# Optimization experiments

Measured on AMD Instinct MI355X. Metric: run time of the kernel, lower is better.

## Reference

```python
import jax, jax.numpy as jnp
import numpy as np
from jax import lax
from math import sqrt

POLE = sqrt(3.0) - 2.0                       # cubic B-spline pole
GAIN = (1.0 - POLE) * (1.0 - 1.0 / POLE)     # = 6.0
UPSAMPLING_FACTOR = 2


def _cubic_spline_1d(t):
    a = jnp.abs(t)
    out = (2.0 / 3.0 + (0.5 * a - 1.0) * a ** 2) * (a < 1)
    out = out + (-(a - 2.0) ** 3 / 6.0) * ((a >= 1) & (a < 2))
    return out


def _bspline_kernel(f):
    is_odd = f % 2
    k = 4 * f - is_odd
    start = (1 + is_odd) / (2 * f) - 2.0
    pts = jnp.arange(k, dtype=jnp.float32) * (1.0 / f) + start
    return _cubic_spline_1d(pts)


def _prefilter_1d(x, axis):
    """Causal + anticausal recursive cubic-spline coefficient filter along `axis`."""
    n = x.shape[axis]
    if n == 1:
        return x
    p = POLE
    xm = jnp.moveaxis(x * GAIN, axis, 0)  # (n, ...)
    i = np.arange(n)
    pows = jnp.asarray(p ** i + p ** (2 * n - 1 - i), dtype=x.dtype)
    # causal boundary condition (mirror)
    c0 = jnp.tensordot(pows, xm, axes=(0, 0)) * (p / (1.0 - p ** (2 * n))) + xm[0]

    def causal(carry, xi):
        y = xi + p * carry
        return y, y

    _, ys = lax.scan(causal, c0, xm[1:])
    cm = jnp.concatenate([c0[None], ys], axis=0)
    # anticausal boundary condition
    last = cm[-1] * (p / (p - 1.0))

    def anti(carry, ci):
        y = p * (carry - ci)
        return y, y

    _, ys2 = lax.scan(anti, last, cm[:-1], reverse=True)
    out = jnp.concatenate([ys2, last[None]], axis=0)
    return jnp.moveaxis(out, 0, axis)


def _upsample_1d(x, axis, kernel, f):
    """Strided transposed conv along `axis` with replicate padding of 2 (per-channel)."""
    dim_size = x.shape[axis]
    xm = jnp.moveaxis(x, axis, -1)
    lead = xm.shape[:-1]
    x3 = xm.reshape(-1, 1, dim_size)
    x3 = jnp.pad(x3, ((0, 0), (0, 0), (2, 2)), mode='edge')
    k = kernel.shape[0]
    implicit_padding = 7 * f // 2
    pad = k - 1 - implicit_padding  # conv_transpose == lhs-dilated correlation w/ flipped kernel
    out = lax.conv_general_dilated(
        x3,
        kernel[::-1][None, None, :],
        window_strides=(1,),
        padding=[(pad, pad)],
        lhs_dilation=(f,),
        dimension_numbers=('NCH', 'OIH', 'NCH'),
    )
    out = out.reshape(lead + (out.shape[-1],))
    return jnp.moveaxis(out, -1, axis)


def setup_inputs() -> dict:
    key = jax.random.key(0)
    volume = jax.random.normal(key, (2, 3, 96, 96, 96), dtype=jnp.float32)
    return {"volume": volume}


def reference(volume):
    f = UPSAMPLING_FACTOR
    kernel = _bspline_kernel(f).astype(volume.dtype)
    first_spatial_dim = min(volume.ndim - 1, 2)
    x = volume
    for axis in range(first_spatial_dim, volume.ndim):
        x = _prefilter_1d(x, axis)
    for axis in range(first_spatial_dim, volume.ndim):
        x = _upsample_1d(x, axis, kernel, f)
    return x
```

## Files before the change

kernel.cpp:

```cpp
#include <hip/hip_runtime.h>


#define TAPS 28

struct MTab { float v[192 * TAPS]; };

static constexpr MTab make_M() {
    const double p = -0.26794919243112270647253365849413;
    double pw[193] = {};
    pw[0] = 1.0;
    for (int i = 1; i <= 192; ++i) pw[i] = pw[i - 1] * p;
    double Wd[96][96] = {};
    for (int j = 0; j < 96; ++j) {
        double c[96] = {};
        double K = p / (1.0 - pw[192]);
        double cur = 6.0 * K * (pw[j] + pw[191 - j]) + (j == 0 ? 6.0 : 0.0);
        c[0] = cur;
        for (int i = 1; i < 96; ++i) {
            cur = (i == j ? 6.0 : 0.0) + p * cur;
            c[i] = cur;
        }
        double nxt = cur * (p / (p - 1.0));
        Wd[95][j] = nxt;
        for (int i = 94; i >= 0; --i) {
            nxt = p * (nxt - c[i]);
            Wd[i][j] = nxt;
        }
    }
    MTab M = {};
    const double cw[8] = {1.0 / 384.0, 121.0 / 384.0, 235.0 / 384.0, 27.0 / 384.0,
                          27.0 / 384.0, 235.0 / 384.0, 121.0 / 384.0, 1.0 / 384.0};
    for (int i = 0; i < 192; ++i) {
        int ph = i & 1;
        int cc = i >> 1;
        for (int t = 0; t < TAPS; ++t) {
            int j = cc - 13 + t;
            double m = 0.0;
            if (j >= 0 && j < 96) {
                for (int tt = 0; tt < 4; ++tt) {
                    int k = cc + ph - 2 + tt;
                    k = k < 0 ? 0 : (k > 95 ? 95 : k);
                    m += cw[ph * 4 + tt] * Wd[k][j];
                }
            }
            M.v[i * TAPS + t] = (float)m;
        }
    }
    return M;
}

static constexpr MTab h_M = make_M();
__device__ __constant__ MTab g_M = h_M;

__device__ alignas(16) float g_bufA[6 * 96 * 96 * 192];
__device__ alignas(16) float g_bufB[6 * 96 * 192 * 192];

__device__ __forceinline__ int clamp96(int j) { return j < 0 ? 0 : (j > 95 ? 95 : j); }

__global__ __launch_bounds__(512) void pass_z(const float* __restrict__ in,
                                              float* __restrict__ out) {
    __shared__ float s_in[64 * 97];
    __shared__ float s_out[64 * 193];
    const float* Mb = g_M.v;
    float w0[TAPS], w1[TAPS];
#pragma unroll
    for (int t = 0; t < TAPS; ++t) {
        w0[t] = Mb[96 * TAPS + t];
        w1[t] = Mb[97 * TAPS + t];
    }
    size_t base = (size_t)blockIdx.x * 64;
    const float* src = in + base * 96;
    int tid = threadIdx.x;
    for (int k = tid; k < 64 * 96; k += 512)
        s_in[(k / 96) * 97 + (k % 96)] = src[k];
    __syncthreads();

    int lane = tid & 63;
    int wave = tid >> 6;
    int c0 = wave * 12;
    const float* xl = s_in + lane * 97;
    float* op = s_out + lane * 193 + 2 * c0;
    float win[39];
#pragma unroll
    for (int k = 0; k < 39; ++k) win[k] = xl[clamp96(c0 - 13 + k)];

    if (wave >= 1 && wave <= 6) {
#pragma unroll
        for (int mi = 0; mi < 12; ++mi) {
            float a0 = 0.f, a1 = 0.f;
#pragma unroll
            for (int t = 0; t < TAPS; ++t) {
                float xv = win[mi + t];
                a0 = fmaf(w0[t], xv, a0);
                a1 = fmaf(w1[t], xv, a1);
            }
            op[2 * mi] = a0;
            op[2 * mi + 1] = a1;
        }
    } else {
#pragma unroll
        for (int mi = 0; mi < 12; ++mi) {
            int m = c0 + mi;
            int wb = __builtin_amdgcn_readfirstlane(m * 2 * TAPS);
            const float* wr = Mb + wb;
            float a0 = 0.f, a1 = 0.f;
#pragma unroll
            for (int t = 0; t < TAPS; ++t) {
                float xv = win[mi + t];
                a0 = fmaf(wr[t], xv, a0);
                a1 = fmaf(wr[TAPS + t], xv, a1);
            }
            op[2 * mi] = a0;
            op[2 * mi + 1] = a1;
        }
    }
    __syncthreads();
    float* dst = out + base * 192;
    for (int k = tid; k < 64 * 192; k += 512)
        dst[k] = s_out[(k / 192) * 193 + (k % 192)];
}

template <int INNER>
__global__ __launch_bounds__(256) void pass_staged(const float* __restrict__ in,
                                                   float* __restrict__ out) {
    constexpr int CT = INNER / 64;
    __shared__ float s[96 * 64];
    const float* Mb = g_M.v;
    int tid = threadIdx.x;
    int ct = blockIdx.x % CT;
    int o = blockIdx.x / CT;
    const float* src = in + (size_t)o * 96 * INNER + (size_t)ct * 64;
    float* dst = out + (size_t)o * 192 * INNER + (size_t)ct * 64;

#pragma unroll
    for (int it = 0; it < 6; ++it) {
        int k = tid + it * 256;
        int row = k >> 4;
        int c4 = k & 15;
        float4 v = *(const float4*)(src + (size_t)row * INNER + c4 * 4);
        *(float4*)(&s[row * 64 + c4 * 4]) = v;
    }
    __syncthreads();

    int col = tid & 63;
    int cq = tid >> 6;
    int c0 = cq * 24;

    float win[51];
#pragma unroll
    for (int k = 0; k < 51; ++k) win[k] = s[clamp96(c0 - 13 + k) * 64 + col];

    if (cq == 1 || cq == 2) {
        float w0[TAPS], w1[TAPS];
#pragma unroll
        for (int t = 0; t < TAPS; ++t) {
            w0[t] = Mb[96 * TAPS + t];
            w1[t] = Mb[97 * TAPS + t];
        }
#pragma unroll
        for (int mi = 0; mi < 24; ++mi) {
            float a0 = 0.f, a1 = 0.f;
#pragma unroll
            for (int t = 0; t < TAPS; ++t) {
                float xv = win[mi + t];
                a0 = fmaf(w0[t], xv, a0);
                a1 = fmaf(w1[t], xv, a1);
            }
            int m = c0 + mi;
            dst[(size_t)(2 * m) * INNER + col] = a0;
            dst[(size_t)(2 * m + 1) * INNER + col] = a1;
        }
    } else {
#pragma unroll
        for (int mi = 0; mi < 24; ++mi) {
            int m = c0 + mi;
            int wb = __builtin_amdgcn_readfirstlane(m * 2 * TAPS);
            const float* wr = Mb + wb;
            float a0 = 0.f, a1 = 0.f;
#pragma unroll
            for (int t = 0; t < TAPS; ++t) {
                float xv = win[mi + t];
                a0 = fmaf(wr[t], xv, a0);
                a1 = fmaf(wr[TAPS + t], xv, a1);
            }
            dst[(size_t)(2 * m) * INNER + col] = a0;
            dst[(size_t)(2 * m + 1) * INNER + col] = a1;
        }
    }
}

extern "C" void kernel_launch(void* const* d_in, const int* in_sizes, int n_in,
                              void* d_out, int out_size, void* d_ws, size_t ws_size,
                              hipStream_t stream) {
    const float* x = (const float*)d_in[0];
    float* out = (float*)d_out;
    float *bufA, *bufB;
    hipGetSymbolAddress((void**)&bufA, HIP_SYMBOL(g_bufA));
    hipGetSymbolAddress((void**)&bufB, HIP_SYMBOL(g_bufB));

    pass_z<<<864, 512, 0, stream>>>(x, bufA);
    pass_staged<192><<<1728, 256, 0, stream>>>(bufA, bufB);
    pass_staged<36864><<<3456, 256, 0, stream>>>(bufB, out);
}
```

Measured before the change: 310.0 us.

## Fuse z and y separable filter passes into one kernel via shared memory

Merges the first two separable passes (along the last and second-to-last axes) into a single kernel. Each block loads a 96x96 plane slice into shared memory, filters along z for 64 output columns into a shared intermediate, then filters along y and writes directly to the y/z-upsampled buffer. This removes the bufA global round trip and one kernel launch. In exchange it recomputes overlapping z halo columns across the three column tiles and uses more shared memory per block, with uneven lane usage (lane<32 branches).

```diff
diff --git a/kernel.cpp b/kernel.cpp
--- a/kernel.cpp
+++ b/kernel.cpp
@@ -52,72 +52,137 @@
 static constexpr MTab h_M = make_M();
 __device__ __constant__ MTab g_M = h_M;
 
-__device__ alignas(16) float g_bufA[6 * 96 * 96 * 192];
 __device__ alignas(16) float g_bufB[6 * 96 * 192 * 192];
 
 __device__ __forceinline__ int clamp96(int j) { return j < 0 ? 0 : (j > 95 ? 95 : j); }
 
-__global__ __launch_bounds__(512) void pass_z(const float* __restrict__ in,
-                                              float* __restrict__ out) {
-    __shared__ float s_in[64 * 97];
-    __shared__ float s_out[64 * 193];
-    const float* Mb = g_M.v;
-    float w0[TAPS], w1[TAPS];
-#pragma unroll
-    for (int t = 0; t < TAPS; ++t) {
-        w0[t] = Mb[96 * TAPS + t];
-        w1[t] = Mb[97 * TAPS + t];
-    }
-    size_t base = (size_t)blockIdx.x * 64;
-    const float* src = in + base * 96;
+__global__ __launch_bounds__(512) void pass_zy(const float* __restrict__ in,
+                                               float* __restrict__ out) {
+    __shared__ float s_in[96 * 65];
+    __shared__ float s_mid[96 * 65];
     int tid = threadIdx.x;
-    for (int k = tid; k < 64 * 96; k += 512)
-        s_in[(k / 96) * 97 + (k % 96)] = src[k];
+    int w = blockIdx.x % 3;
+    int oa = blockIdx.x / 3;
+    const float* src = in + (size_t)oa * 96 * 96;
+    float* dst = out + (size_t)oa * 192 * 192 + 64 * w;
+    int jlo = 32 * w - 13;
+
+#pragma unroll
+    for (int it = 0; it < 12; ++it) {
+        int k = tid + it * 512;
+        int b = k >> 6;
+        int zi = k & 63;
+        s_in[b * 65 + zi] = src[b * 96 + clamp96(jlo + zi)];
+    }
     __syncthreads();
 
     int lane = tid & 63;
-    int wave = tid >> 6;
-    int c0 = wave * 12;
-    const float* xl = s_in + lane * 97;
-    float* op = s_out + lane * 193 + 2 * c0;
-    float win[39];
-#pragma unroll
-    for (int k = 0; k < 39; ++k) win[k] = xl[clamp96(c0 - 13 + k)];
-
-    if (wave >= 1 && wave <= 6) {
-#pragma unroll
-        for (int mi = 0; mi < 12; ++mi) {
-            float a0 = 0.f, a1 = 0.f;
+    int wv = tid >> 6;
+
+    {
+        float w0[TAPS], w1[TAPS];
+#pragma unroll
+        for (int t = 0; t < TAPS; ++t) {
+            w0[t] = g_M.v[96 * TAPS + t];
+            w1[t] = g_M.v[97 * TAPS + t];
+        }
+        float win1[31], win2[31];
+        const float* p1 = s_in + lane * 65 + 4 * wv;
+#pragma unroll
+        for (int k = 0; k < 31; ++k) win1[k] = p1[k];
+        if (lane < 32) {
+            const float* p2 = s_in + (lane + 64) * 65 + 4 * wv;
+#pragma unroll
+            for (int k = 0; k < 31; ++k) win2[k] = p2[k];
+        }
+        float* q1 = s_mid + lane * 65 + 8 * wv;
+        float* q2 = s_mid + (lane + 64) * 65 + 8 * wv;
+#pragma unroll
+        for (int mi = 0; mi < 4; ++mi) {
+            int m_g = 32 * w + 4 * wv + mi;
+            float a0 = 0.f, a1 = 0.f, c0v = 0.f, c1v = 0.f;
+            if (m_g >= 12 && m_g < 84) {
+#pragma unroll
+                for (int t = 0; t < TAPS; ++t) {
+                    a0 = fmaf(w0[t], win1[mi + t], a0);
+                    a1 = fmaf(w1[t], win1[mi + t], a1);
+                }
+                if (lane < 32) {
+#pragma unroll
+                    for (int t = 0; t < TAPS; ++t) {
+                        c0v = fmaf(w0[t], win2[mi + t], c0v);
+                        c1v = fmaf(w1[t], win2[mi + t], c1v);
+                    }
+                }
+            } else {
+                int wb = __builtin_amdgcn_readfirstlane(m_g * 2 * TAPS);
+                const float* wr = g_M.v + wb;
+#pragma unroll
+                for (int t = 0; t < TAPS; ++t) {
+                    a0 = fmaf(wr[t], win1[mi + t], a0);
+                    a1 = fmaf(wr[TAPS + t], win1[mi + t], a1);
+                }
+                if (lane < 32) {
+#pragma unroll
+                    for (int t = 0; t < TAPS; ++t) {
+                        c0v = fmaf(wr[t], win2[mi + t], c0v);
+                        c1v = fmaf(wr[TAPS + t], win2[mi + t], c1v);
+                    }
+                }
+            }
+            q1[2 * mi] = a0;
+            q1[2 * mi + 1] = a1;
+            if (lane < 32) {
+                q2[2 * mi] = c0v;
+                q2[2 * mi + 1] = c1v;
+            }
+        }
+    }
+    __syncthreads();
+
+    {
+        int c0 = 12 * wv;
+        float win[39];
+#pragma unroll
+        for (int k = 0; k < 39; ++k) win[k] = s_mid[clamp96(c0 - 13 + k) * 65 + lane];
+        if (wv >= 1 && wv <= 6) {
+            float w0[TAPS], w1[TAPS];
 #pragma unroll
             for (int t = 0; t < TAPS; ++t) {
-                float xv = win[mi + t];
-                a0 = fmaf(w0[t], xv, a0);
-                a1 = fmaf(w1[t], xv, a1);
-            }
-            op[2 * mi] = a0;
-            op[2 * mi + 1] = a1;
-        }
-    } else {
-#pragma unroll
-        for (int mi = 0; mi < 12; ++mi) {
-            int m = c0 + mi;
-            int wb = __builtin_amdgcn_readfirstlane(m * 2 * TAPS);
-            const float* wr = Mb + wb;
-            float a0 = 0.f, a1 = 0.f;
-#pragma unroll
-            for (int t = 0; t < TAPS; ++t) {
-                float xv = win[mi + t];
-                a0 = fmaf(wr[t], xv, a0);
-                a1 = fmaf(wr[TAPS + t], xv, a1);
-            }
-            op[2 * mi] = a0;
-            op[2 * mi + 1] = a1;
-        }
-    }
-    __syncthreads();
-    float* dst = out + base * 192;
-    for (int k = tid; k < 64 * 192; k += 512)
-        dst[k] = s_out[(k / 192) * 193 + (k % 192)];
+                w0[t] = g_M.v[96 * TAPS + t];
+                w1[t] = g_M.v[97 * TAPS + t];
+            }
+#pragma unroll
+            for (int mi = 0; mi < 12; ++mi) {
+                float a0 = 0.f, a1 = 0.f;
+#pragma unroll
+                for (int t = 0; t < TAPS; ++t) {
+                    float xv = win[mi + t];
+                    a0 = fmaf(w0[t], xv, a0);
+                    a1 = fmaf(w1[t], xv, a1);
+                }
+                int c = c0 + mi;
+                dst[(size_t)(2 * c) * 192 + lane] = a0;
+                dst[(size_t)(2 * c + 1) * 192 + lane] = a1;
+            }
+        } else {
+#pragma unroll
+            for (int mi = 0; mi < 12; ++mi) {
+                int c = c0 + mi;
+                int wb = __builtin_amdgcn_readfirstlane(c * 2 * TAPS);
+                const float* wr = g_M.v + wb;
+                float a0 = 0.f, a1 = 0.f;
+#pragma unroll
+                for (int t = 0; t < TAPS; ++t) {
+                    float xv = win[mi + t];
+                    a0 = fmaf(wr[t], xv, a0);
+                    a1 = fmaf(wr[TAPS + t], xv, a1);
+                }
+                dst[(size_t)(2 * c) * 192 + lane] = a0;
+                dst[(size_t)(2 * c + 1) * 192 + lane] = a1;
+            }
+        }
+    }
 }
 
 template <int INNER>
@@ -194,11 +259,9 @@
                               hipStream_t stream) {
     const float* x = (const float*)d_in[0];
     float* out = (float*)d_out;
-    float *bufA, *bufB;
-    hipGetSymbolAddress((void**)&bufA, HIP_SYMBOL(g_bufA));
+    float* bufB;
     hipGetSymbolAddress((void**)&bufB, HIP_SYMBOL(g_bufB));
 
-    pass_z<<<864, 512, 0, stream>>>(x, bufA);
-    pass_staged<192><<<1728, 256, 0, stream>>>(bufA, bufB);
+    pass_zy<<<1728, 512, 0, stream>>>(x, bufB);
     pass_staged<36864><<<3456, 256, 0, stream>>>(bufB, out);
 }
```

Measured after the change: 284.5 us. 8.2% less time.
